# Kernel tuning notes

Hardware: AMD Instinct MI355X
Metric: run time of the kernel (lower is better)

## Reference

```python
import math
import jax, jax.numpy as jnp
import numpy as np

STRIDE = 8
IMG = 2048
NA = 9            # num anchors per cell (len(cfg['anchor_size']))
NC = 80           # num classes
TOPK = 1000
CONF = 0.05
NMS_T = 0.6
CTR_CLAMP = 32.0
EXP_CLAMP = math.log(1e8)            # DEFAULT_EXP_CLAMP
SCALE_CLAMP = math.log(1000.0 / 16)  # DEFAULT_SCALE_CLAMP


def setup_inputs() -> dict:
    key = jax.random.key(0)
    k1, k2, k3 = jax.random.split(key, 3)
    H = W = IMG // STRIDE  # 256
    obj_pred = jax.random.normal(k1, (1, NA, H, W), jnp.float32)
    cls_pred = jax.random.normal(k2, (1, NA * NC, H, W), jnp.float32)
    reg_pred = jax.random.normal(k3, (1, NA * 4, H, W), jnp.float32) * 0.5
    # generate_anchors: grid centers (+0.5)*stride, tiled anchor sizes -> [H*W*NA, 4] (cx,cy,w,h)
    ys, xs = jnp.meshgrid(jnp.arange(H), jnp.arange(W), indexing='ij')
    xy = (jnp.stack([xs, ys], -1).reshape(-1, 2).astype(jnp.float32) + 0.5) * STRIDE
    sizes = jnp.array([[32, 32], [64, 64], [128, 128], [32, 64], [64, 128],
                       [128, 256], [64, 32], [128, 64], [256, 128]], jnp.float32)
    anchor_boxes = jnp.concatenate(
        [jnp.repeat(xy[:, None, :], NA, axis=1),
         jnp.broadcast_to(sizes[None], (H * W, NA, 2))], axis=-1).reshape(-1, 4)
    return {"obj_pred": obj_pred, "cls_pred": cls_pred,
            "reg_pred": reg_pred, "anchor_boxes": anchor_boxes}


def _detect(obj_pred, cls_pred, reg_pred, anchor_boxes):
    B, _, H, W = obj_pred.shape
    obj = obj_pred.reshape(B, NA, 1, H, W)
    cls = cls_pred.reshape(B, NA, NC, H, W)
    # normalized_cls_pred = cls + obj - log(1 + exp(clamp(cls)) + exp(clamp(obj)))
    norm = cls + obj - jnp.log(1.0 + jnp.exp(jnp.minimum(cls, EXP_CLAMP))
                               + jnp.exp(jnp.minimum(obj, EXP_CLAMP)))
    norm = norm.transpose(0, 3, 4, 1, 2).reshape(B, -1, NC)[0]          # [M, NC]
    reg = reg_pred.reshape(B, NA, 4, H, W).transpose(0, 3, 4, 1, 2).reshape(B, -1, 4)[0]  # [M, 4]
    prob = jax.nn.sigmoid(norm)
    scores_all = prob.max(axis=-1)
    labels_all = prob.argmax(axis=-1)
    scores, idx = jax.lax.top_k(scores_all, TOPK)                        # descending
    labels = labels_all[idx]
    reg = reg[idx]
    anc = anchor_boxes[idx]
    # decode_boxes
    ctr_off = jnp.clip(reg[..., :2] * anc[..., 2:], -CTR_CLAMP, CTR_CLAMP)
    ctr = anc[..., :2] + ctr_off
    wh = anc[..., 2:] * jnp.exp(jnp.minimum(reg[..., 2:], SCALE_CLAMP))
    boxes = jnp.concatenate([ctr - 0.5 * wh, ctr + 0.5 * wh], axis=-1)
    boxes = jnp.clip(boxes / IMG, 0.0, 1.0)
    return scores, labels, boxes


def _nms_keep(scores, labels, boxes):
    # scores are sorted descending; per-class greedy NMS == class-masked global greedy NMS
    valid = scores >= CONF
    x1, y1, x2, y2 = boxes[:, 0], boxes[:, 1], boxes[:, 2], boxes[:, 3]
    areas = (x2 - x1) * (y2 - y1)
    xx1 = jnp.maximum(x1[:, None], x1[None, :])
    yy1 = jnp.maximum(y1[:, None], y1[None, :])
    xx2 = jnp.minimum(x2[:, None], x2[None, :])
    yy2 = jnp.minimum(y2[:, None], y2[None, :])
    inter = jnp.maximum(1e-28, xx2 - xx1) * jnp.maximum(1e-28, yy2 - yy1)
    iou = inter / (areas[:, None] + areas[None, :] - inter + 1e-14)      # [N, N]
    sup = (iou > NMS_T) & (labels[:, None] == labels[None, :])
    later = jnp.arange(TOPK)[None, :] > jnp.arange(TOPK)[:, None]

    def body(i, keep):
        row = sup[i] & later[i] & keep[i]   # i suppresses only if still kept
        return keep & ~row

    return jax.lax.fori_loop(0, TOPK, body, valid)


def reference(obj_pred, cls_pred, reg_pred, anchor_boxes):
    scores, labels, boxes = _detect(obj_pred, cls_pred, reg_pred, anchor_boxes)
    keep = _nms_keep(scores, labels, boxes)
    # fixed-shape outputs: detections sorted by score with a keep mask
    return scores, labels, boxes, keep
```

## Files before the change

### kernel.cpp

```cpp
#include <hip/hip_runtime.h>
#include <stdint.h>

#define NA 9
#define NC 80
#define NTOT 589824
#define TOPK 1000
#define CONF 0.05f
#define NMS_T 0.6
#define CTR_CLAMP 32.0
#define IMGF 2048.0
#define SCALE_CLAMP 4.135166556742356

#define BITS_OFF   0u
#define LABELS_OFF 2359296u
#define HIST_OFF   4718592u
#define CNT_OFF    4784128u
#define CUTB_OFF   4784132u
#define CAND_OFF   4784384u
#define BOXES_OFF  4817152u
#define LABS_OFF   4833152u
#define SUPB_OFF   4837376u

__device__ __forceinline__ float cexpf(float x) {
#pragma clang fp contract(off)
  float m = floorf(__builtin_fmaf(x, 1.44269504088896341f, 0.5f));
  float r = __builtin_fmaf(m, -0.693359375f, x);
  r = __builtin_fmaf(m, 2.12194440e-4f, r);
  float r2 = r * r;
  float y = 1.9875691500E-4f;
  y = __builtin_fmaf(y, r, 1.3981999507E-3f);
  y = __builtin_fmaf(y, r, 8.3334519073E-3f);
  y = __builtin_fmaf(y, r, 4.1665795894E-2f);
  y = __builtin_fmaf(y, r, 1.6666665459E-1f);
  y = __builtin_fmaf(y, r, 5.0000001201E-1f);
  y = __builtin_fmaf(y, r2, r) + 1.0f;
  return ldexpf(y, (int)m);
}

__device__ __forceinline__ float clogf_(float xin) {
#pragma clang fp contract(off)
  unsigned b = __float_as_uint(xin);
  int e = (int)(b >> 23) - 126;
  float m = __uint_as_float((b & 0x007FFFFFu) | 0x3F000000u);
  if (m < 0.707106781186547524f) { e -= 1; m = m + m; }
  float x = m - 1.0f;
  float z = x * x;
  float y = 7.0376836292E-2f;
  y = __builtin_fmaf(y, x, -1.1514610310E-1f);
  y = __builtin_fmaf(y, x, 1.1676998740E-1f);
  y = __builtin_fmaf(y, x, -1.2420140846E-1f);
  y = __builtin_fmaf(y, x, 1.4249322787E-1f);
  y = __builtin_fmaf(y, x, -1.6668057665E-1f);
  y = __builtin_fmaf(y, x, 2.0000714765E-1f);
  y = __builtin_fmaf(y, x, -2.4999993993E-1f);
  y = __builtin_fmaf(y, x, 3.3333331174E-1f);
  y = y * x * z;
  float ef = (float)e;
  y = __builtin_fmaf(ef, -2.12194440e-4f, y);
  y = __builtin_fmaf(-0.5f, z, y);
  float res = x + y;
  res = __builtin_fmaf(ef, 0.693359375f, res);
  return res;
}

__global__ __launch_bounds__(256) void k_score(const float4* __restrict__ obj4,
                                               const float4* __restrict__ cls4,
                                               unsigned* __restrict__ bits_all,
                                               int* __restrict__ labels_all,
                                               unsigned* __restrict__ hist) {
#pragma clang fp contract(off)
  __shared__ unsigned lh[16384];
  int tid = threadIdx.x;
  for (int b = tid; b < 16384; b += 256) lh[b] = 0u;
  __syncthreads();
  int t = blockIdx.x * 256 + tid;
  int a = t >> 14;
  int rem = t & 16383;
  float4 ov = obj4[t];
  float ob[4] = {ov.x, ov.y, ov.z, ov.w};
  float best[4] = {-1e30f, -1e30f, -1e30f, -1e30f};
  int bc[4] = {0, 0, 0, 0};
  const float4* cp = cls4 + a * 80 * 16384 + rem;
#pragma unroll 8
  for (int c = 0; c < 80; c++) {
    float4 cv = cp[c * 16384];
    float cl[4] = {cv.x, cv.y, cv.z, cv.w};
#pragma unroll
    for (int k = 0; k < 4; k++) {
      if (cl[k] > best[k]) { best[k] = cl[k]; bc[k] = c; }
    }
  }
  unsigned bv[4];
#pragma unroll
  for (int k = 0; k < 4; k++) {
    float c = best[k], o = ob[k];
    float ec = cexpf(c);
    float eo = cexpf(o);
    float L = clogf_((1.0f + ec) + eo);
    float nrm = (c + o) - L;
    float p = 1.0f / (1.0f + cexpf(-nrm));
    bv[k] = __float_as_uint(p);
    atomicAdd(&lh[bv[k] >> 16], 1u);
  }
  unsigned po = (unsigned)(a * 65536 + rem * 4);
#pragma unroll
  for (int k = 0; k < 4; k++) { bits_all[po + k] = bv[k]; labels_all[po + k] = bc[k]; }
  __syncthreads();
  for (int b = tid; b < 16384; b += 256) {
    unsigned v = lh[b];
    if (v) atomicAdd(&hist[b], v);
  }
}

__global__ __launch_bounds__(1024) void k_cutoff(const unsigned* __restrict__ hist,
                                                 unsigned* __restrict__ cutB) {
  __shared__ unsigned suf[1024];
  __shared__ int sC;
  __shared__ unsigned sAbove;
  int tid = threadIdx.x;
  unsigned s = 0;
  for (int b = 0; b < 16; b++) s += hist[tid * 16 + b];
  unsigned v = s;
  suf[tid] = v;
  __syncthreads();
  for (int off = 1; off < 1024; off <<= 1) {
    unsigned add = (tid + off < 1024) ? suf[tid + off] : 0u;
    __syncthreads();
    v += add;
    suf[tid] = v;
    __syncthreads();
  }
  unsigned nxt = (tid < 1023) ? suf[tid + 1] : 0u;
  if (v >= TOPK && nxt < TOPK) { sC = tid; sAbove = nxt; }
  __syncthreads();
  int C = sC;
  unsigned above = sAbove;
  if (tid < 16) {
    unsigned acc = above;
    for (int b = 15; b >= tid; b--) acc += hist[C * 16 + b];
    unsigned h = hist[C * 16 + tid];
    if (acc >= TOPK && (tid == 15 || (acc - h) < TOPK)) *cutB = (unsigned)(C * 16 + tid);
  }
}

__global__ __launch_bounds__(256) void k_compact(const unsigned* __restrict__ bits_all,
                                                 const unsigned* __restrict__ cutB,
                                                 unsigned* __restrict__ cand_cnt,
                                                 unsigned long long* __restrict__ cand) {
  unsigned t = blockIdx.x * 256 + threadIdx.x;
  unsigned bits = bits_all[t];
  bool win = (bits >> 16) >= *cutB;
  unsigned long long m = __ballot(win);
  if (m == 0ull) return;
  int lane = threadIdx.x & 63;
  int leader = __ffsll((long long)m) - 1;
  unsigned base = 0;
  if (lane == leader) base = atomicAdd(cand_cnt, (unsigned)__popcll(m));
  base = __shfl(base, leader, 64);
  if (win) {
    unsigned a = t >> 16;
    unsigned hw = t & 65535u;
    unsigned j = hw * 9u + a;
    unsigned pos = base + (unsigned)__popcll(m & ((1ull << lane) - 1ull));
    if (pos < 4096u)
      cand[pos] = ((unsigned long long)bits << 20) | (unsigned long long)(0xFFFFFu - j);
  }
}

__global__ __launch_bounds__(256) void k_rank(const unsigned* __restrict__ cand_cnt,
                                              const unsigned long long* __restrict__ cand,
                                              const int* __restrict__ labels_all,
                                              const float* __restrict__ reg_pred,
                                              const float* __restrict__ anchors,
                                              float* __restrict__ out,
                                              float* __restrict__ boxes_s,
                                              int* __restrict__ labels_s) {
  __shared__ unsigned long long lkey[256];
  int tid = threadIdx.x;
  int c = blockIdx.x * 256 + tid;
  unsigned M = *cand_cnt;
  if (M > 4096u) M = 4096u;
  unsigned long long mykey = (c < (int)M) ? cand[c] : 0ull;
  unsigned rank = 0;
  for (int tile = 0; tile < 16; tile++) {
    __syncthreads();
    int src = tile * 256 + tid;
    lkey[tid] = (src < (int)M) ? cand[src] : 0ull;
    __syncthreads();
#pragma unroll 8
    for (int q = 0; q < 256; q++) rank += (lkey[q] > mykey) ? 1u : 0u;
  }
  if (c < (int)M && rank < TOPK) {
    int r = (int)rank;
    unsigned j = 0xFFFFFu - (unsigned)(mykey & 0xFFFFFull);
    unsigned hw = j / 9u;
    unsigned a = j - hw * 9u;
    int lab = labels_all[a * 65536u + hw];
    unsigned base = a * 4u * 65536u + hw;
    double r0 = (double)reg_pred[base];
    double r1 = (double)reg_pred[base + 65536u];
    double r2 = (double)reg_pred[base + 131072u];
    double r3 = (double)reg_pred[base + 196608u];
    double ax = (double)anchors[j * 4u + 0], ay = (double)anchors[j * 4u + 1];
    double aw = (double)anchors[j * 4u + 2], ah = (double)anchors[j * 4u + 3];
    double ox = fmin(fmax(r0 * aw, -CTR_CLAMP), CTR_CLAMP);
    double oy = fmin(fmax(r1 * ah, -CTR_CLAMP), CTR_CLAMP);
    double cx = ax + ox, cy = ay + oy;
    double ww = aw * exp(fmin(r2, SCALE_CLAMP));
    double hh = ah * exp(fmin(r3, SCALE_CLAMP));
    float x1 = (float)fmin(fmax((cx - 0.5 * ww) * (1.0 / IMGF), 0.0), 1.0);
    float y1 = (float)fmin(fmax((cy - 0.5 * hh) * (1.0 / IMGF), 0.0), 1.0);
    float x2 = (float)fmin(fmax((cx + 0.5 * ww) * (1.0 / IMGF), 0.0), 1.0);
    float y2 = (float)fmin(fmax((cy + 0.5 * hh) * (1.0 / IMGF), 0.0), 1.0);
    out[r] = __uint_as_float((unsigned)(mykey >> 20));
    out[1000 + r] = (float)lab;
    out[2000 + 4 * r + 0] = x1;
    out[2000 + 4 * r + 1] = y1;
    out[2000 + 4 * r + 2] = x2;
    out[2000 + 4 * r + 3] = y2;
    boxes_s[4 * r + 0] = x1;
    boxes_s[4 * r + 1] = y1;
    boxes_s[4 * r + 2] = x2;
    boxes_s[4 * r + 3] = y2;
    labels_s[r] = lab;
  }
}

__global__ __launch_bounds__(256) void k_sup(const float* __restrict__ boxes_s,
                                             const int* __restrict__ labels_s,
                                             unsigned long long* __restrict__ supB) {
  __shared__ float bx[4000];
  __shared__ int lb[1000];
  int i = blockIdx.x;
  int tid = threadIdx.x;
  for (int t = tid; t < 4000; t += 256) bx[t] = boxes_s[t];
  for (int t = tid; t < 1000; t += 256) lb[t] = labels_s[t];
  __syncthreads();
  double ix1 = (double)bx[4 * i], iy1 = (double)bx[4 * i + 1];
  double ix2 = (double)bx[4 * i + 2], iy2 = (double)bx[4 * i + 3];
  double ia = (ix2 - ix1) * (iy2 - iy1);
  int il = lb[i];
  for (int rep = 0; rep < 4; rep++) {
    int j = rep * 256 + tid;
    bool s = false;
    if (j < TOPK && j > i && lb[j] == il) {
      double jx1 = (double)bx[4 * j], jy1 = (double)bx[4 * j + 1];
      double jx2 = (double)bx[4 * j + 2], jy2 = (double)bx[4 * j + 3];
      double xx1 = fmax(ix1, jx1), yy1 = fmax(iy1, jy1);
      double xx2 = fmin(ix2, jx2), yy2 = fmin(iy2, jy2);
      double inter = fmax(1e-28, xx2 - xx1) * fmax(1e-28, yy2 - yy1);
      double ja = (jx2 - jx1) * (jy2 - jy1);
      double iou = inter / (ia + ja - inter + 1e-14);
      s = iou > NMS_T;
    }
    unsigned long long w = __ballot(s);
    if ((tid & 63) == 0) supB[(rep * 4 + (tid >> 6)) * 1024 + i] = w;
  }
}

__device__ __forceinline__ unsigned long long shflxor64(unsigned long long v, int m) {
  unsigned lo = __shfl_xor((unsigned)v, m, 64);
  unsigned hi = __shfl_xor((unsigned)(v >> 32), m, 64);
  return ((unsigned long long)hi << 32) | lo;
}

__global__ __launch_bounds__(64) void k_nms(const unsigned long long* __restrict__ supB,
                                            const float* __restrict__ scores,
                                            float* __restrict__ keep_out) {
  int lane = threadIdx.x;
  unsigned long long inval[16];
#pragma unroll
  for (int m = 0; m < 16; m++) {
    int j = m * 64 + lane;
    bool bad = (j >= TOPK) || (scores[j] < CONF);
    inval[m] = __ballot(bad);
  }
  unsigned long long kept[16];
#pragma unroll
  for (int b = 0; b < 16; b++) {
    unsigned long long acc = 0ull;
#pragma unroll
    for (int m = 0; m < b; m++) {
      unsigned long long r = supB[b * 1024 + m * 64 + lane];
      if ((kept[m] >> lane) & 1ull) acc |= r;
    }
    if (b > 0) {
#pragma unroll
      for (int s = 1; s < 64; s <<= 1) acc |= shflxor64(acc, s);
    }
    unsigned alo = __builtin_amdgcn_readfirstlane((unsigned)acc);
    unsigned ahi = __builtin_amdgcn_readfirstlane((unsigned)(acc >> 32));
    unsigned long long cur = inval[b] | (((unsigned long long)ahi << 32) | alo);
    unsigned long long diag = supB[b * 1024 + b * 64 + lane];
    unsigned dlo = (unsigned)diag, dhi = (unsigned)(diag >> 32);
#pragma unroll 8
    for (int k = 0; k < 64; k++) {
      unsigned rlo = __builtin_amdgcn_readlane(dlo, k);
      unsigned rhi = __builtin_amdgcn_readlane(dhi, k);
      unsigned long long rk = ((unsigned long long)rhi << 32) | rlo;
      unsigned long long take = ((cur >> k) & 1ull) ? 0ull : rk;
      cur |= take;
    }
    kept[b] = ~cur;
  }
#pragma unroll
  for (int m = 0; m < 16; m++) {
    int j = m * 64 + lane;
    if (j < TOPK) keep_out[j] = ((kept[m] >> lane) & 1ull) ? 1.0f : 0.0f;
  }
}

extern "C" void kernel_launch(void* const* d_in, const int* in_sizes, int n_in,
                              void* d_out, int out_size, void* d_ws, size_t ws_size,
                              hipStream_t stream) {
  const float* obj = (const float*)d_in[0];
  const float* cls = (const float*)d_in[1];
  const float* reg = (const float*)d_in[2];
  const float* anc = (const float*)d_in[3];
  float* out = (float*)d_out;
  char* ws = (char*)d_ws;

  unsigned* bits_all = (unsigned*)(ws + BITS_OFF);
  int* labels_all = (int*)(ws + LABELS_OFF);
  unsigned* hist = (unsigned*)(ws + HIST_OFF);
  unsigned* cand_cnt = (unsigned*)(ws + CNT_OFF);
  unsigned* cutB = (unsigned*)(ws + CUTB_OFF);
  unsigned long long* cand = (unsigned long long*)(ws + CAND_OFF);
  float* boxes_s = (float*)(ws + BOXES_OFF);
  int* labels_s = (int*)(ws + LABS_OFF);
  unsigned long long* supB = (unsigned long long*)(ws + SUPB_OFF);

  hipMemsetAsync(ws + HIST_OFF, 0, 65536 + 512, stream);

  k_score<<<576, 256, 0, stream>>>((const float4*)obj, (const float4*)cls, bits_all, labels_all, hist);
  k_cutoff<<<1, 1024, 0, stream>>>(hist, cutB);
  k_compact<<<2304, 256, 0, stream>>>(bits_all, cutB, cand_cnt, cand);
  k_rank<<<16, 256, 0, stream>>>(cand_cnt, cand, labels_all, reg, anc, out, boxes_s, labels_s);
  k_sup<<<1000, 256, 0, stream>>>(boxes_s, labels_s, supB);
  k_nms<<<1, 64, 0, stream>>>(supB, out, out + 6000);
}
```

Before: 435.8 us.

## Fuse post-scoring stages into one cooperative kernel with grid syncs

Replaces the cutoff, compact, rank, suppression-matrix and NMS kernels with a single cooperative kernel of 512 blocks that uses grid-wide syncs between phases. The goal is to remove the launch gaps between five small kernels. The rank phase also stops scanning tiles beyond the real candidate count. In exchange, grid.sync barriers add their own cost, and idle blocks wait through the serial single-block phases.

```diff
diff --git a/kernel.cpp b/kernel.cpp
--- a/kernel.cpp
+++ b/kernel.cpp
@@ -1,5 +1,8 @@
 #include <hip/hip_runtime.h>
+#include <hip/hip_cooperative_groups.h>
 #include <stdint.h>
+
+namespace cg = cooperative_groups;
 
 #define NA 9
 #define NC 80
@@ -112,201 +115,222 @@
   }
 }
 
-__global__ __launch_bounds__(1024) void k_cutoff(const unsigned* __restrict__ hist,
-                                                 unsigned* __restrict__ cutB) {
-  __shared__ unsigned suf[1024];
-  __shared__ int sC;
-  __shared__ unsigned sAbove;
-  int tid = threadIdx.x;
-  unsigned s = 0;
-  for (int b = 0; b < 16; b++) s += hist[tid * 16 + b];
-  unsigned v = s;
-  suf[tid] = v;
-  __syncthreads();
-  for (int off = 1; off < 1024; off <<= 1) {
-    unsigned add = (tid + off < 1024) ? suf[tid + off] : 0u;
-    __syncthreads();
-    v += add;
-    suf[tid] = v;
-    __syncthreads();
-  }
-  unsigned nxt = (tid < 1023) ? suf[tid + 1] : 0u;
-  if (v >= TOPK && nxt < TOPK) { sC = tid; sAbove = nxt; }
-  __syncthreads();
-  int C = sC;
-  unsigned above = sAbove;
-  if (tid < 16) {
-    unsigned acc = above;
-    for (int b = 15; b >= tid; b--) acc += hist[C * 16 + b];
-    unsigned h = hist[C * 16 + tid];
-    if (acc >= TOPK && (tid == 15 || (acc - h) < TOPK)) *cutB = (unsigned)(C * 16 + tid);
-  }
-}
-
-__global__ __launch_bounds__(256) void k_compact(const unsigned* __restrict__ bits_all,
-                                                 const unsigned* __restrict__ cutB,
-                                                 unsigned* __restrict__ cand_cnt,
-                                                 unsigned long long* __restrict__ cand) {
-  unsigned t = blockIdx.x * 256 + threadIdx.x;
-  unsigned bits = bits_all[t];
-  bool win = (bits >> 16) >= *cutB;
-  unsigned long long m = __ballot(win);
-  if (m == 0ull) return;
-  int lane = threadIdx.x & 63;
-  int leader = __ffsll((long long)m) - 1;
-  unsigned base = 0;
-  if (lane == leader) base = atomicAdd(cand_cnt, (unsigned)__popcll(m));
-  base = __shfl(base, leader, 64);
-  if (win) {
-    unsigned a = t >> 16;
-    unsigned hw = t & 65535u;
-    unsigned j = hw * 9u + a;
-    unsigned pos = base + (unsigned)__popcll(m & ((1ull << lane) - 1ull));
-    if (pos < 4096u)
-      cand[pos] = ((unsigned long long)bits << 20) | (unsigned long long)(0xFFFFFu - j);
-  }
-}
-
-__global__ __launch_bounds__(256) void k_rank(const unsigned* __restrict__ cand_cnt,
-                                              const unsigned long long* __restrict__ cand,
-                                              const int* __restrict__ labels_all,
-                                              const float* __restrict__ reg_pred,
-                                              const float* __restrict__ anchors,
-                                              float* __restrict__ out,
-                                              float* __restrict__ boxes_s,
-                                              int* __restrict__ labels_s) {
-  __shared__ unsigned long long lkey[256];
-  int tid = threadIdx.x;
-  int c = blockIdx.x * 256 + tid;
-  unsigned M = *cand_cnt;
-  if (M > 4096u) M = 4096u;
-  unsigned long long mykey = (c < (int)M) ? cand[c] : 0ull;
-  unsigned rank = 0;
-  for (int tile = 0; tile < 16; tile++) {
-    __syncthreads();
-    int src = tile * 256 + tid;
-    lkey[tid] = (src < (int)M) ? cand[src] : 0ull;
-    __syncthreads();
-#pragma unroll 8
-    for (int q = 0; q < 256; q++) rank += (lkey[q] > mykey) ? 1u : 0u;
-  }
-  if (c < (int)M && rank < TOPK) {
-    int r = (int)rank;
-    unsigned j = 0xFFFFFu - (unsigned)(mykey & 0xFFFFFull);
-    unsigned hw = j / 9u;
-    unsigned a = j - hw * 9u;
-    int lab = labels_all[a * 65536u + hw];
-    unsigned base = a * 4u * 65536u + hw;
-    double r0 = (double)reg_pred[base];
-    double r1 = (double)reg_pred[base + 65536u];
-    double r2 = (double)reg_pred[base + 131072u];
-    double r3 = (double)reg_pred[base + 196608u];
-    double ax = (double)anchors[j * 4u + 0], ay = (double)anchors[j * 4u + 1];
-    double aw = (double)anchors[j * 4u + 2], ah = (double)anchors[j * 4u + 3];
-    double ox = fmin(fmax(r0 * aw, -CTR_CLAMP), CTR_CLAMP);
-    double oy = fmin(fmax(r1 * ah, -CTR_CLAMP), CTR_CLAMP);
-    double cx = ax + ox, cy = ay + oy;
-    double ww = aw * exp(fmin(r2, SCALE_CLAMP));
-    double hh = ah * exp(fmin(r3, SCALE_CLAMP));
-    float x1 = (float)fmin(fmax((cx - 0.5 * ww) * (1.0 / IMGF), 0.0), 1.0);
-    float y1 = (float)fmin(fmax((cy - 0.5 * hh) * (1.0 / IMGF), 0.0), 1.0);
-    float x2 = (float)fmin(fmax((cx + 0.5 * ww) * (1.0 / IMGF), 0.0), 1.0);
-    float y2 = (float)fmin(fmax((cy + 0.5 * hh) * (1.0 / IMGF), 0.0), 1.0);
-    out[r] = __uint_as_float((unsigned)(mykey >> 20));
-    out[1000 + r] = (float)lab;
-    out[2000 + 4 * r + 0] = x1;
-    out[2000 + 4 * r + 1] = y1;
-    out[2000 + 4 * r + 2] = x2;
-    out[2000 + 4 * r + 3] = y2;
-    boxes_s[4 * r + 0] = x1;
-    boxes_s[4 * r + 1] = y1;
-    boxes_s[4 * r + 2] = x2;
-    boxes_s[4 * r + 3] = y2;
-    labels_s[r] = lab;
-  }
-}
-
-__global__ __launch_bounds__(256) void k_sup(const float* __restrict__ boxes_s,
-                                             const int* __restrict__ labels_s,
-                                             unsigned long long* __restrict__ supB) {
-  __shared__ float bx[4000];
-  __shared__ int lb[1000];
-  int i = blockIdx.x;
-  int tid = threadIdx.x;
-  for (int t = tid; t < 4000; t += 256) bx[t] = boxes_s[t];
-  for (int t = tid; t < 1000; t += 256) lb[t] = labels_s[t];
-  __syncthreads();
-  double ix1 = (double)bx[4 * i], iy1 = (double)bx[4 * i + 1];
-  double ix2 = (double)bx[4 * i + 2], iy2 = (double)bx[4 * i + 3];
-  double ia = (ix2 - ix1) * (iy2 - iy1);
-  int il = lb[i];
-  for (int rep = 0; rep < 4; rep++) {
-    int j = rep * 256 + tid;
-    bool s = false;
-    if (j < TOPK && j > i && lb[j] == il) {
-      double jx1 = (double)bx[4 * j], jy1 = (double)bx[4 * j + 1];
-      double jx2 = (double)bx[4 * j + 2], jy2 = (double)bx[4 * j + 3];
-      double xx1 = fmax(ix1, jx1), yy1 = fmax(iy1, jy1);
-      double xx2 = fmin(ix2, jx2), yy2 = fmin(iy2, jy2);
-      double inter = fmax(1e-28, xx2 - xx1) * fmax(1e-28, yy2 - yy1);
-      double ja = (jx2 - jx1) * (jy2 - jy1);
-      double iou = inter / (ia + ja - inter + 1e-14);
-      s = iou > NMS_T;
-    }
-    unsigned long long w = __ballot(s);
-    if ((tid & 63) == 0) supB[(rep * 4 + (tid >> 6)) * 1024 + i] = w;
-  }
-}
-
 __device__ __forceinline__ unsigned long long shflxor64(unsigned long long v, int m) {
   unsigned lo = __shfl_xor((unsigned)v, m, 64);
   unsigned hi = __shfl_xor((unsigned)(v >> 32), m, 64);
   return ((unsigned long long)hi << 32) | lo;
 }
 
-__global__ __launch_bounds__(64) void k_nms(const unsigned long long* __restrict__ supB,
-                                            const float* __restrict__ scores,
-                                            float* __restrict__ keep_out) {
-  int lane = threadIdx.x;
-  unsigned long long inval[16];
-#pragma unroll
-  for (int m = 0; m < 16; m++) {
-    int j = m * 64 + lane;
-    bool bad = (j >= TOPK) || (scores[j] < CONF);
-    inval[m] = __ballot(bad);
-  }
-  unsigned long long kept[16];
-#pragma unroll
-  for (int b = 0; b < 16; b++) {
-    unsigned long long acc = 0ull;
-#pragma unroll
-    for (int m = 0; m < b; m++) {
-      unsigned long long r = supB[b * 1024 + m * 64 + lane];
-      if ((kept[m] >> lane) & 1ull) acc |= r;
-    }
-    if (b > 0) {
-#pragma unroll
-      for (int s = 1; s < 64; s <<= 1) acc |= shflxor64(acc, s);
-    }
-    unsigned alo = __builtin_amdgcn_readfirstlane((unsigned)acc);
-    unsigned ahi = __builtin_amdgcn_readfirstlane((unsigned)(acc >> 32));
-    unsigned long long cur = inval[b] | (((unsigned long long)ahi << 32) | alo);
-    unsigned long long diag = supB[b * 1024 + b * 64 + lane];
-    unsigned dlo = (unsigned)diag, dhi = (unsigned)(diag >> 32);
+__global__ __launch_bounds__(256) void k_tail(const unsigned* __restrict__ hist,
+                                              const unsigned* __restrict__ bits_all,
+                                              const int* __restrict__ labels_all,
+                                              const float* __restrict__ reg_pred,
+                                              const float* __restrict__ anchors,
+                                              unsigned* __restrict__ cutB,
+                                              unsigned* __restrict__ cand_cnt,
+                                              unsigned long long* __restrict__ cand,
+                                              float* __restrict__ out,
+                                              float* __restrict__ boxes_s,
+                                              int* __restrict__ labels_s,
+                                              unsigned long long* __restrict__ supB) {
+  cg::grid_group grid = cg::this_grid();
+  int tid = threadIdx.x;
+  int bid = blockIdx.x;
+
+  __shared__ __align__(16) char smem[20032];
+  unsigned* s_cut = (unsigned*)smem;
+  unsigned long long* s_key = (unsigned long long*)smem;
+  float* s_bx = (float*)smem;
+  int* s_lb = (int*)(smem + 16000);
+  __shared__ int sC;
+  __shared__ unsigned sAbove;
+
+  if (bid == 0) {
+    unsigned base = (unsigned)tid * 64u;
+    unsigned s = 0;
+    for (int b = 0; b < 64; b++) s += hist[base + b];
+    unsigned v = s;
+    s_cut[tid] = v;
+    __syncthreads();
+    for (int off = 1; off < 256; off <<= 1) {
+      unsigned add = (tid + off < 256) ? s_cut[tid + off] : 0u;
+      __syncthreads();
+      v += add;
+      s_cut[tid] = v;
+      __syncthreads();
+    }
+    unsigned nxt = (tid < 255) ? s_cut[tid + 1] : 0u;
+    if (v >= TOPK && nxt < TOPK) { sC = tid; sAbove = nxt; }
+    __syncthreads();
+    int C = sC;
+    unsigned above = sAbove;
+    if (tid < 64) {
+      unsigned h = hist[(unsigned)C * 64u + (unsigned)tid];
+      unsigned acc = h;
+      for (int off = 1; off < 64; off <<= 1) {
+        unsigned o = __shfl_down(acc, off, 64);
+        if (tid + off < 64) acc += o;
+      }
+      acc += above;
+      if (acc >= TOPK && (tid == 63 || (acc - h) < TOPK))
+        *cutB = (unsigned)(C * 64 + tid);
+    }
+  }
+  grid.sync();
+
+  {
+    unsigned cB = *cutB;
+    for (unsigned t = (unsigned)bid * 256u + (unsigned)tid; t < (unsigned)NTOT;
+         t += 131072u) {
+      unsigned bits = bits_all[t];
+      bool win = (bits >> 16) >= cB;
+      unsigned long long m = __ballot(win);
+      if (m != 0ull) {
+        int lane = tid & 63;
+        int leader = __ffsll((long long)m) - 1;
+        unsigned base2 = 0;
+        if (lane == leader) base2 = atomicAdd(cand_cnt, (unsigned)__popcll(m));
+        base2 = __shfl(base2, leader, 64);
+        if (win) {
+          unsigned a = t >> 16;
+          unsigned hw = t & 65535u;
+          unsigned j = hw * 9u + a;
+          unsigned pos = base2 + (unsigned)__popcll(m & ((1ull << lane) - 1ull));
+          if (pos < 4096u)
+            cand[pos] = ((unsigned long long)bits << 20) |
+                        (unsigned long long)(0xFFFFFu - j);
+        }
+      }
+    }
+  }
+  grid.sync();
+
+  if (bid < 16) {
+    int c = bid * 256 + tid;
+    unsigned M = *cand_cnt;
+    if (M > 4096u) M = 4096u;
+    unsigned long long mykey = (c < (int)M) ? cand[c] : 0ull;
+    unsigned rank = 0;
+    int ntile = (int)((M + 255u) >> 8);
+    for (int tile = 0; tile < ntile; tile++) {
+      __syncthreads();
+      int src = tile * 256 + tid;
+      s_key[tid] = (src < (int)M) ? cand[src] : 0ull;
+      __syncthreads();
 #pragma unroll 8
-    for (int k = 0; k < 64; k++) {
-      unsigned rlo = __builtin_amdgcn_readlane(dlo, k);
-      unsigned rhi = __builtin_amdgcn_readlane(dhi, k);
-      unsigned long long rk = ((unsigned long long)rhi << 32) | rlo;
-      unsigned long long take = ((cur >> k) & 1ull) ? 0ull : rk;
-      cur |= take;
-    }
-    kept[b] = ~cur;
-  }
-#pragma unroll
-  for (int m = 0; m < 16; m++) {
-    int j = m * 64 + lane;
-    if (j < TOPK) keep_out[j] = ((kept[m] >> lane) & 1ull) ? 1.0f : 0.0f;
+      for (int q = 0; q < 256; q++) rank += (s_key[q] > mykey) ? 1u : 0u;
+    }
+    if (c < (int)M && rank < TOPK) {
+      int r = (int)rank;
+      unsigned j = 0xFFFFFu - (unsigned)(mykey & 0xFFFFFull);
+      unsigned hw = j / 9u;
+      unsigned a = j - hw * 9u;
+      int lab = labels_all[a * 65536u + hw];
+      unsigned base = a * 4u * 65536u + hw;
+      double r0 = (double)reg_pred[base];
+      double r1 = (double)reg_pred[base + 65536u];
+      double r2 = (double)reg_pred[base + 131072u];
+      double r3 = (double)reg_pred[base + 196608u];
+      double ax = (double)anchors[j * 4u + 0], ay = (double)anchors[j * 4u + 1];
+      double aw = (double)anchors[j * 4u + 2], ah = (double)anchors[j * 4u + 3];
+      double ox = fmin(fmax(r0 * aw, -CTR_CLAMP), CTR_CLAMP);
+      double oy = fmin(fmax(r1 * ah, -CTR_CLAMP), CTR_CLAMP);
+      double cx = ax + ox, cy = ay + oy;
+      double ww = aw * exp(fmin(r2, SCALE_CLAMP));
+      double hh = ah * exp(fmin(r3, SCALE_CLAMP));
+      float x1 = (float)fmin(fmax((cx - 0.5 * ww) * (1.0 / IMGF), 0.0), 1.0);
+      float y1 = (float)fmin(fmax((cy - 0.5 * hh) * (1.0 / IMGF), 0.0), 1.0);
+      float x2 = (float)fmin(fmax((cx + 0.5 * ww) * (1.0 / IMGF), 0.0), 1.0);
+      float y2 = (float)fmin(fmax((cy + 0.5 * hh) * (1.0 / IMGF), 0.0), 1.0);
+      out[r] = __uint_as_float((unsigned)(mykey >> 20));
+      out[1000 + r] = (float)lab;
+      out[2000 + 4 * r + 0] = x1;
+      out[2000 + 4 * r + 1] = y1;
+      out[2000 + 4 * r + 2] = x2;
+      out[2000 + 4 * r + 3] = y2;
+      boxes_s[4 * r + 0] = x1;
+      boxes_s[4 * r + 1] = y1;
+      boxes_s[4 * r + 2] = x2;
+      boxes_s[4 * r + 3] = y2;
+      labels_s[r] = lab;
+    }
+  }
+  grid.sync();
+
+  for (int t = tid; t < 4000; t += 256) s_bx[t] = boxes_s[t];
+  for (int t = tid; t < 1000; t += 256) s_lb[t] = labels_s[t];
+  __syncthreads();
+  for (int half = 0; half < 2; half++) {
+    int i = bid + half * 512;
+    if (i < TOPK) {
+      double ix1 = (double)s_bx[4 * i], iy1 = (double)s_bx[4 * i + 1];
+      double ix2 = (double)s_bx[4 * i + 2], iy2 = (double)s_bx[4 * i + 3];
+      double ia = (ix2 - ix1) * (iy2 - iy1);
+      int il = s_lb[i];
+      for (int rep = 0; rep < 4; rep++) {
+        int j = rep * 256 + tid;
+        bool s = false;
+        if (j < TOPK && j > i && s_lb[j] == il) {
+          double jx1 = (double)s_bx[4 * j], jy1 = (double)s_bx[4 * j + 1];
+          double jx2 = (double)s_bx[4 * j + 2], jy2 = (double)s_bx[4 * j + 3];
+          double xx1 = fmax(ix1, jx1), yy1 = fmax(iy1, jy1);
+          double xx2 = fmin(ix2, jx2), yy2 = fmin(iy2, jy2);
+          double inter = fmax(1e-28, xx2 - xx1) * fmax(1e-28, yy2 - yy1);
+          double ja = (jx2 - jx1) * (jy2 - jy1);
+          double iou = inter / (ia + ja - inter + 1e-14);
+          s = iou > NMS_T;
+        }
+        unsigned long long w = __ballot(s);
+        if ((tid & 63) == 0) supB[(rep * 4 + (tid >> 6)) * 1024 + i] = w;
+      }
+    }
+  }
+  grid.sync();
+
+  if (bid == 0 && tid < 64) {
+    int lane = tid;
+    const float* scores = out;
+    float* keep_out = out + 6000;
+    unsigned long long inval[16];
+#pragma unroll
+    for (int m = 0; m < 16; m++) {
+      int j = m * 64 + lane;
+      bool bad = (j >= TOPK) || (scores[j] < CONF);
+      inval[m] = __ballot(bad);
+    }
+    unsigned long long kept[16];
+#pragma unroll
+    for (int b = 0; b < 16; b++) {
+      unsigned long long acc = 0ull;
+#pragma unroll
+      for (int m = 0; m < b; m++) {
+        unsigned long long r = supB[b * 1024 + m * 64 + lane];
+        if ((kept[m] >> lane) & 1ull) acc |= r;
+      }
+      if (b > 0) {
+#pragma unroll
+        for (int s = 1; s < 64; s <<= 1) acc |= shflxor64(acc, s);
+      }
+      unsigned alo = __builtin_amdgcn_readfirstlane((unsigned)acc);
+      unsigned ahi = __builtin_amdgcn_readfirstlane((unsigned)(acc >> 32));
+      unsigned long long cur = inval[b] | (((unsigned long long)ahi << 32) | alo);
+      unsigned long long diag = supB[b * 1024 + b * 64 + lane];
+      unsigned dlo = (unsigned)diag, dhi = (unsigned)(diag >> 32);
+#pragma unroll 8
+      for (int k = 0; k < 64; k++) {
+        unsigned rlo = __builtin_amdgcn_readlane(dlo, k);
+        unsigned rhi = __builtin_amdgcn_readlane(dhi, k);
+        unsigned long long rk = ((unsigned long long)rhi << 32) | rlo;
+        unsigned long long take = ((cur >> k) & 1ull) ? 0ull : rk;
+        cur |= take;
+      }
+      kept[b] = ~cur;
+    }
+#pragma unroll
+    for (int m = 0; m < 16; m++) {
+      int j = m * 64 + lane;
+      if (j < TOPK) keep_out[j] = ((kept[m] >> lane) & 1ull) ? 1.0f : 0.0f;
+    }
   }
 }
 
@@ -332,10 +356,13 @@
 
   hipMemsetAsync(ws + HIST_OFF, 0, 65536 + 512, stream);
 
-  k_score<<<576, 256, 0, stream>>>((const float4*)obj, (const float4*)cls, bits_all, labels_all, hist);
-  k_cutoff<<<1, 1024, 0, stream>>>(hist, cutB);
-  k_compact<<<2304, 256, 0, stream>>>(bits_all, cutB, cand_cnt, cand);
-  k_rank<<<16, 256, 0, stream>>>(cand_cnt, cand, labels_all, reg, anc, out, boxes_s, labels_s);
-  k_sup<<<1000, 256, 0, stream>>>(boxes_s, labels_s, supB);
-  k_nms<<<1, 64, 0, stream>>>(supB, out, out + 6000);
-}
+  k_score<<<576, 256, 0, stream>>>((const float4*)obj, (const float4*)cls, bits_all,
+                                   labels_all, hist);
+
+  void* kargs[] = {(void*)&hist,    (void*)&bits_all, (void*)&labels_all,
+                   (void*)&reg,     (void*)&anc,      (void*)&cutB,
+                   (void*)&cand_cnt, (void*)&cand,    (void*)&out,
+                   (void*)&boxes_s, (void*)&labels_s, (void*)&supB};
+  hipLaunchCooperativeKernel((const void*)k_tail, dim3(512), dim3(256), kargs, 0,
+                             stream);
+}
```

Result: slower. 603.8 us (+38.6%).
